# Optimization experiments

Hardware: AMD Instinct MI355X
Metric: run time of the kernel (lower is better)

Reference implementation:

```python
import jax, jax.numpy as jnp
import numpy as np

N_NODES = 100000
EPS = 1e-12  # F.normalize eps


def mean_aggregate(x, src, dst):
    # gather source features along edges, segment-mean into destinations
    msg = x[src]                                              # [E, D]
    summed = jax.ops.segment_sum(msg, dst, num_segments=N_NODES)  # [N, D]
    cnt = jax.ops.segment_sum(jnp.ones_like(dst, dtype=x.dtype), dst,
                              num_segments=N_NODES)           # [N]
    return summed / jnp.maximum(cnt, 1.0)[:, None]


def sage_conv(x, src, dst, W_l, b_l, W_r, normalize):
    agg = mean_aggregate(x, src, dst)
    out = agg @ W_l.T + b_l + x @ W_r.T  # lin_l(mean neigh) + lin_r(root)
    if normalize:
        norm = jnp.sqrt(jnp.sum(out * out, axis=-1, keepdims=True))
        out = out / jnp.maximum(norm, EPS)
    return out


def setup_inputs() -> dict:
    key = jax.random.key(0)
    ks = jax.random.split(key, 8)
    H, O = 128, 128
    s = 1.0 / np.sqrt(H)
    x = jax.random.normal(ks[0], (N_NODES, H), dtype=jnp.float32)
    edge_index = jax.random.randint(ks[1], (2, 1600000), 0, N_NODES, dtype=jnp.int64)
    return {
        "x": x,
        "edge_index": edge_index,
        "W1l": jax.random.uniform(ks[2], (H, H), jnp.float32, -s, s),
        "b1": jax.random.uniform(ks[3], (H,), jnp.float32, -s, s),
        "W1r": jax.random.uniform(ks[4], (H, H), jnp.float32, -s, s),
        "W2l": jax.random.uniform(ks[5], (O, H), jnp.float32, -s, s),
        "b2": jax.random.uniform(ks[6], (O,), jnp.float32, -s, s),
        "W2r": jax.random.uniform(ks[7], (O, H), jnp.float32, -s, s),
    }


def reference(x, edge_index, W1l, b1, W1r, W2l, b2, W2r):
    src, dst = edge_index[0], edge_index[1]
    h = sage_conv(x, src, dst, W1l, b1, W1r, normalize=True)
    h = jax.nn.relu(h)
    out = sage_conv(h, src, dst, W2l, b2, W2r, normalize=False)
    return out
```

## Files before the change

kernel.cpp:

```cpp
#include <hip/hip_runtime.h>
#include <hip/hip_bf16.h>
#include <hip/hip_fp16.h>

#define N_NODES 100000
#define DFEAT 128
#define SLAB 4096
#define BSHIFT 9
#define NBUCK 196

#define WS_CNT      0
#define WS_GH       100000
#define WS_PARTB    180000
#define WS_OFFS     200000
#define WS_ESRC     300608
#define WS_AGGH     1900608
#define WS_CASTH    8300608

typedef _Float16 half8 __attribute__((ext_vector_type(8)));
typedef _Float16 half2v __attribute__((ext_vector_type(2)));
typedef float floatx4 __attribute__((ext_vector_type(4)));

__global__ __launch_bounds__(256) void prep_kernel(const float* __restrict__ x,
                                                   __half* __restrict__ xh, int total4,
                                                   const int* __restrict__ dst,
                                                   int* __restrict__ gh,
                                                   int E, int bpart, int castblocks) {
    __shared__ int lh[NBUCK];
    int b = blockIdx.x;
    if (b < castblocks) {
        int i = b * 256 + threadIdx.x;
        if (i < total4) {
            float4 v = ((const float4*)x)[i];
            __half2 h01 = __floats2half2_rn(v.x, v.y);
            __half2 h23 = __floats2half2_rn(v.z, v.w);
            uint2 o;
            o.x = *(unsigned int*)&h01;
            o.y = *(unsigned int*)&h23;
            ((uint2*)xh)[i] = o;
        }
        return;
    }
    int bb = b - castblocks;
    for (int i = threadIdx.x; i < NBUCK; i += 256) lh[i] = 0;
    __syncthreads();
    int s0 = bb * SLAB, s1 = min(E, s0 + SLAB);
    for (int i = s0 + threadIdx.x; i < s1; i += 256)
        atomicAdd(&lh[dst[i] >> BSHIFT], 1);
    __syncthreads();
    for (int i = threadIdx.x; i < NBUCK; i += 256) gh[i * bpart + bb] = lh[i];
}

__global__ void scan1_kernel(int* __restrict__ gh, int* __restrict__ partial, int m) {
    __shared__ int s[256];
    int i = blockIdx.x * 256 + threadIdx.x;
    int v = (i < m) ? gh[i] : 0;
    s[threadIdx.x] = v;
    __syncthreads();
    for (int d = 1; d < 256; d <<= 1) {
        int t = (threadIdx.x >= d) ? s[threadIdx.x - d] : 0;
        __syncthreads();
        s[threadIdx.x] += t;
        __syncthreads();
    }
    int incl = s[threadIdx.x];
    if (i < m) gh[i] = incl - v;
    if (threadIdx.x == 255) partial[blockIdx.x] = incl;
}

__global__ void scan2_kernel(int* __restrict__ partial, int nb) {
    __shared__ int s[512];
    int t = threadIdx.x;
    int v = (t < nb) ? partial[t] : 0;
    s[t] = v;
    __syncthreads();
    for (int d = 1; d < 512; d <<= 1) {
        int u = (t >= d) ? s[t - d] : 0;
        __syncthreads();
        s[t] += u;
        __syncthreads();
    }
    if (t < nb) partial[t] = s[t] - v;
}

__global__ void scan3_kernel(int* __restrict__ gh, const int* __restrict__ partial, int m) {
    int i = blockIdx.x * 256 + threadIdx.x;
    if (i < m) gh[i] += partial[blockIdx.x];
}

__global__ __launch_bounds__(256) void phase2_kernel(const int* __restrict__ src,
                                                     const int* __restrict__ dst,
                                                     const int* __restrict__ gbase,
                                                     int2* __restrict__ pairs,
                                                     int E, int bpart) {
    __shared__ int lbase[NBUCK];
    __shared__ int lcur[NBUCK];
    __shared__ int lgb[NBUCK];
    __shared__ int sc[256];
    __shared__ int2 lp[SLAB];
    int b = blockIdx.x;
    int t = threadIdx.x;
    for (int i = t; i < NBUCK; i += 256) lbase[i] = 0;
    __syncthreads();
    int s0 = b * SLAB, s1 = min(E, s0 + SLAB);
    for (int i = s0 + t; i < s1; i += 256)
        atomicAdd(&lbase[dst[i] >> BSHIFT], 1);
    __syncthreads();
    int v = (t < NBUCK) ? lbase[t] : 0;
    sc[t] = v;
    __syncthreads();
    for (int d = 1; d < 256; d <<= 1) {
        int u = (t >= d) ? sc[t - d] : 0;
        __syncthreads();
        sc[t] += u;
        __syncthreads();
    }
    if (t < NBUCK) {
        int excl = sc[t] - v;
        lbase[t] = excl;
        lcur[t] = excl;
        lgb[t] = gbase[t * bpart + b];
    }
    __syncthreads();
    for (int i = s0 + t; i < s1; i += 256) {
        int d = dst[i];
        int s = src[i];
        int bk = d >> BSHIFT;
        int pos = atomicAdd(&lcur[bk], 1);
        lp[pos] = make_int2(s, d);
    }
    __syncthreads();
    int m = s1 - s0;
    for (int i = t; i < m; i += 256) {
        int2 p = lp[i];
        int bk = p.y >> BSHIFT;
        pairs[lgb[bk] + (i - lbase[bk])] = p;
    }
}

__global__ __launch_bounds__(512) void phase3_kernel(const int2* __restrict__ pairs,
                                                     const int* __restrict__ gbase,
                                                     int* __restrict__ cnt,
                                                     int* __restrict__ offs,
                                                     int* __restrict__ esrc,
                                                     int E, int bpart, int n) {
    __shared__ int lcnt[512];
    __shared__ int sc[512];
    __shared__ int lexcl[512];
    int g = blockIdx.x;
    int node0 = g << BSHIFT;
    int t = threadIdx.x;
    lcnt[t] = 0;
    __syncthreads();
    int S = gbase[g * bpart];
    int Eg = (g == NBUCK - 1) ? E : gbase[(g + 1) * bpart];
    for (int i = S + t; i < Eg; i += 512)
        atomicAdd(&lcnt[pairs[i].y - node0], 1);
    __syncthreads();
    int v = lcnt[t];
    sc[t] = v;
    __syncthreads();
    for (int d = 1; d < 512; d <<= 1) {
        int u = (t >= d) ? sc[t - d] : 0;
        __syncthreads();
        sc[t] += u;
        __syncthreads();
    }
    int excl = sc[t] - v;
    lexcl[t] = excl;
    int nd = node0 + t;
    if (nd < n) {
        cnt[nd] = v;
        offs[nd] = S + excl;
    }
    __syncthreads();
    for (int i = S + t; i < Eg; i += 512) {
        int2 p = pairs[i];
        int pos = atomicAdd(&lexcl[p.y - node0], 1);
        esrc[S + pos] = p.x;
    }
}

#define ACC(c, r)                        \
    s[c][0] += *(half2v*)&(r).x;         \
    s[c][1] += *(half2v*)&(r).y;         \
    s[c][2] += *(half2v*)&(r).z;         \
    s[c][3] += *(half2v*)&(r).w;

__global__ void aggregate_kernel(const __half* __restrict__ feat, const int* __restrict__ esrc,
                                 const int* __restrict__ offs, const int* __restrict__ cnt,
                                 __half* __restrict__ agg, int n) {
    int wid = (blockIdx.x * blockDim.x + threadIdx.x) >> 6;
    int lane = threadIdx.x & 63;
    int grp = lane >> 4;
    int l15 = lane & 15;
    int node = wid * 4 + grp;
    if (node >= n) return;
    int beg = offs[node];
    int deg = cnt[node];
    const _Float16* fbase = (const _Float16*)feat + l15 * 8;
    const int* ep = esrc + beg;

    half2v s[4][4];
#pragma unroll
    for (int c = 0; c < 4; c++)
#pragma unroll
        for (int k = 0; k < 4; k++) s[c][k] = (half2v)(_Float16)0;

    int j = 0;
    for (; j + 8 <= deg; j += 8) {
        int i0 = ep[j + 0], i1 = ep[j + 1], i2 = ep[j + 2], i3 = ep[j + 3];
        int i4 = ep[j + 4], i5 = ep[j + 5], i6 = ep[j + 6], i7 = ep[j + 7];
        uint4 r0 = *(const uint4*)(fbase + (size_t)i0 * DFEAT);
        uint4 r1 = *(const uint4*)(fbase + (size_t)i1 * DFEAT);
        uint4 r2 = *(const uint4*)(fbase + (size_t)i2 * DFEAT);
        uint4 r3 = *(const uint4*)(fbase + (size_t)i3 * DFEAT);
        uint4 r4 = *(const uint4*)(fbase + (size_t)i4 * DFEAT);
        uint4 r5 = *(const uint4*)(fbase + (size_t)i5 * DFEAT);
        uint4 r6 = *(const uint4*)(fbase + (size_t)i6 * DFEAT);
        uint4 r7 = *(const uint4*)(fbase + (size_t)i7 * DFEAT);
        ACC(0, r0) ACC(1, r1) ACC(2, r2) ACC(3, r3)
        ACC(0, r4) ACC(1, r5) ACC(2, r6) ACC(3, r7)
    }
    for (; j + 4 <= deg; j += 4) {
        int i0 = ep[j + 0], i1 = ep[j + 1], i2 = ep[j + 2], i3 = ep[j + 3];
        uint4 r0 = *(const uint4*)(fbase + (size_t)i0 * DFEAT);
        uint4 r1 = *(const uint4*)(fbase + (size_t)i1 * DFEAT);
        uint4 r2 = *(const uint4*)(fbase + (size_t)i2 * DFEAT);
        uint4 r3 = *(const uint4*)(fbase + (size_t)i3 * DFEAT);
        ACC(0, r0) ACC(1, r1) ACC(2, r2) ACC(3, r3)
    }
    if (j < deg) {
        int rem = deg - j;
        int i0 = ep[j];
        int i1 = ep[j + (rem > 1 ? 1 : 0)];
        int i2 = ep[j + (rem > 2 ? 2 : 0)];
        uint4 r0 = *(const uint4*)(fbase + (size_t)i0 * DFEAT);
        uint4 r1 = *(const uint4*)(fbase + (size_t)i1 * DFEAT);
        uint4 r2 = *(const uint4*)(fbase + (size_t)i2 * DFEAT);
        if (rem < 2) { r1.x = 0u; r1.y = 0u; r1.z = 0u; r1.w = 0u; }
        if (rem < 3) { r2.x = 0u; r2.y = 0u; r2.z = 0u; r2.w = 0u; }
        ACC(0, r0) ACC(1, r1) ACC(2, r2)
    }

    float scale = 1.0f / fmaxf((float)deg, 1.0f);
    float a[8];
#pragma unroll
    for (int k = 0; k < 4; k++) {
        a[2 * k]     = ((float)s[0][k].x + (float)s[1][k].x) + ((float)s[2][k].x + (float)s[3][k].x);
        a[2 * k + 1] = ((float)s[0][k].y + (float)s[1][k].y) + ((float)s[2][k].y + (float)s[3][k].y);
    }
    __half2 h0 = __floats2half2_rn(a[0] * scale, a[1] * scale);
    __half2 h1 = __floats2half2_rn(a[2] * scale, a[3] * scale);
    __half2 h2 = __floats2half2_rn(a[4] * scale, a[5] * scale);
    __half2 h3 = __floats2half2_rn(a[6] * scale, a[7] * scale);
    uint4 o;
    o.x = *(unsigned int*)&h0;
    o.y = *(unsigned int*)&h1;
    o.z = *(unsigned int*)&h2;
    o.w = *(unsigned int*)&h3;
    *(uint4*)(agg + (size_t)node * DFEAT + l15 * 8) = o;
}

template <bool NORM_RELU>
__global__ __launch_bounds__(256) void gemm_mfma_kernel(
    const __half* __restrict__ A1_, const __half* __restrict__ A2_,
    const float* __restrict__ Wl, const float* __restrict__ Wr,
    const float* __restrict__ bias, float* __restrict__ out32,
    __half* __restrict__ out16, int n) {
    __shared__ __align__(16) _Float16 lw[128 * 136];

    const _Float16* A1 = (const _Float16*)A1_;
    const _Float16* A2 = (const _Float16*)A2_;

    const int lane = threadIdx.x & 63;
    const int w = threadIdx.x >> 6;
    const int quad = lane >> 4;
    const int l15 = lane & 15;
    const int i0 = blockIdx.x * 128 + w * 32;

    floatx4 acc[2][8];
#pragma unroll
    for (int nt = 0; nt < 2; nt++)
#pragma unroll
        for (int ft = 0; ft < 8; ft++)
            acc[nt][ft] = (floatx4){0.f, 0.f, 0.f, 0.f};

    int r0 = i0 + l15;      if (r0 >= n) r0 = n - 1;
    int r1 = i0 + 16 + l15; if (r1 >= n) r1 = n - 1;
    const int kq = quad * 8;

    for (int half = 0; half < 2; half++) {
        const float* __restrict__ W = half ? Wr : Wl;
        const _Float16* __restrict__ A = half ? A2 : A1;
        if (half) __syncthreads();
        {
            int t = threadIdx.x;
            int row = t >> 1;
            int cb = (t & 1) * 64;
            const float4* sp = (const float4*)(W + row * DFEAT + cb);
            unsigned int* dp = (unsigned int*)&lw[row * 136 + cb];
#pragma unroll
            for (int q = 0; q < 16; q++) {
                float4 v = sp[q];
                __half2 h01 = __floats2half2_rn(v.x, v.y);
                __half2 h23 = __floats2half2_rn(v.z, v.w);
                dp[q * 2] = *(unsigned int*)&h01;
                dp[q * 2 + 1] = *(unsigned int*)&h23;
            }
        }
        __syncthreads();
#pragma unroll
        for (int kc = 0; kc < DFEAT; kc += 32) {
            half8 b0 = *(const half8*)(A + (size_t)r0 * DFEAT + kc + kq);
            half8 b1 = *(const half8*)(A + (size_t)r1 * DFEAT + kc + kq);
#pragma unroll
            for (int ft = 0; ft < 8; ft++) {
                half8 a = *(const half8*)&lw[(ft * 16 + l15) * 136 + kc + kq];
                acc[0][ft] = __builtin_amdgcn_mfma_f32_16x16x32_f16(a, b0, acc[0][ft], 0, 0, 0);
                acc[1][ft] = __builtin_amdgcn_mfma_f32_16x16x32_f16(a, b1, acc[1][ft], 0, 0, 0);
            }
        }
    }

#pragma unroll
    for (int nt = 0; nt < 2; nt++) {
        int node = i0 + nt * 16 + l15;
        float v[8][4];
#pragma unroll
        for (int ft = 0; ft < 8; ft++) {
            const float4 bq = *(const float4*)(bias + ft * 16 + quad * 4);
            v[ft][0] = acc[nt][ft][0] + bq.x;
            v[ft][1] = acc[nt][ft][1] + bq.y;
            v[ft][2] = acc[nt][ft][2] + bq.z;
            v[ft][3] = acc[nt][ft][3] + bq.w;
        }
        if (NORM_RELU) {
            float ss = 0.f;
#pragma unroll
            for (int ft = 0; ft < 8; ft++)
#pragma unroll
                for (int r = 0; r < 4; r++) ss = fmaf(v[ft][r], v[ft][r], ss);
            ss += __shfl_xor(ss, 16);
            ss += __shfl_xor(ss, 32);
            float inv = 1.0f / fmaxf(sqrtf(ss), 1e-12f);
#pragma unroll
            for (int ft = 0; ft < 8; ft++)
#pragma unroll
                for (int r = 0; r < 4; r++) v[ft][r] = fmaxf(v[ft][r] * inv, 0.0f);
        }
        if (node < n) {
            if (NORM_RELU) {
                __half* op = (__half*)out16 + (size_t)node * DFEAT + quad * 4;
#pragma unroll
                for (int ft = 0; ft < 8; ft++) {
                    __half2 h01 = __floats2half2_rn(v[ft][0], v[ft][1]);
                    __half2 h23 = __floats2half2_rn(v[ft][2], v[ft][3]);
                    uint2 o;
                    o.x = *(unsigned int*)&h01;
                    o.y = *(unsigned int*)&h23;
                    *(uint2*)(op + ft * 16) = o;
                }
            } else {
                float* op = out32 + (size_t)node * DFEAT + quad * 4;
#pragma unroll
                for (int ft = 0; ft < 8; ft++)
                    *(float4*)(op + ft * 16) = make_float4(v[ft][0], v[ft][1], v[ft][2], v[ft][3]);
            }
        }
    }
}

extern "C" void kernel_launch(void* const* d_in, const int* in_sizes, int n_in,
                              void* d_out, int out_size, void* d_ws, size_t ws_size,
                              hipStream_t stream) {
    const float* x = (const float*)d_in[0];
    const int* edge_index = (const int*)d_in[1];
    const float* W1l = (const float*)d_in[2];
    const float* b1 = (const float*)d_in[3];
    const float* W1r = (const float*)d_in[4];
    const float* W2l = (const float*)d_in[5];
    const float* b2 = (const float*)d_in[6];
    const float* W2r = (const float*)d_in[7];
    float* out = (float*)d_out;

    const int E = in_sizes[1] / 2;
    const int n = in_sizes[0] / DFEAT;

    int* ws = (int*)d_ws;
    int* cnt = ws + WS_CNT;
    int* gh = ws + WS_GH;
    int* partialB = ws + WS_PARTB;
    int* offs = ws + WS_OFFS;
    int* esrc = ws + WS_ESRC;
    int2* pairs = (int2*)(ws + WS_AGGH);
    __half* aggh = (__half*)(ws + WS_AGGH);
    __half* casth = (__half*)(ws + WS_CASTH);

    const int* src = edge_index;
    const int* dst = edge_index + E;

    const int bpart = (E + SLAB - 1) / SLAB;
    const int m = NBUCK * bpart;
    const int blocksB = (m + 255) / 256;
    const int total4 = n * DFEAT / 4;
    const int castblocks = (total4 + 255) / 256;

    prep_kernel<<<castblocks + bpart, 256, 0, stream>>>(x, casth, total4, dst, gh,
                                                        E, bpart, castblocks);
    scan1_kernel<<<blocksB, 256, 0, stream>>>(gh, partialB, m);
    scan2_kernel<<<1, 512, 0, stream>>>(partialB, blocksB);
    scan3_kernel<<<blocksB, 256, 0, stream>>>(gh, partialB, m);

    phase2_kernel<<<bpart, 256, 0, stream>>>(src, dst, gh, pairs, E, bpart);
    phase3_kernel<<<NBUCK, 512, 0, stream>>>(pairs, gh, cnt, offs, esrc, E, bpart, n);

    const int nwaves = (n + 3) / 4;
    const int aggb = (nwaves * 64 + 255) / 256;
    const int gemmb = (n + 127) / 128;

    aggregate_kernel<<<aggb, 256, 0, stream>>>(casth, esrc, offs, cnt, aggh, n);
    gemm_mfma_kernel<true><<<gemmb, 256, 0, stream>>>(aggh, casth, W1l, W1r, b1, nullptr, aggh, n);

    aggregate_kernel<<<aggb, 256, 0, stream>>>(aggh, esrc, offs, cnt, casth, n);
    gemm_mfma_kernel<false><<<gemmb, 256, 0, stream>>>(casth, aggh, W2l, W2r, b2, out, nullptr, n);
}
```

Before: 346.2 us.

## Replace per-slab bucket scan with atomic bucket bases and pre-cast fp16 weights

```diff
diff --git a/kernel.cpp b/kernel.cpp
--- a/kernel.cpp
+++ b/kernel.cpp
@@ -9,8 +9,10 @@
 #define NBUCK 196
 
 #define WS_CNT      0
-#define WS_GH       100000
-#define WS_PARTB    180000
+#define WS_W16      100000
+#define WS_BCNT     180000
+#define WS_BBASE    180200
+#define WS_BCUR     180400
 #define WS_OFFS     200000
 #define WS_ESRC     300608
 #define WS_AGGH     1900608
@@ -23,7 +25,12 @@
 __global__ __launch_bounds__(256) void prep_kernel(const float* __restrict__ x,
                                                    __half* __restrict__ xh, int total4,
                                                    const int* __restrict__ dst,
-                                                   int* __restrict__ gh,
+                                                   int* __restrict__ bcnt,
+                                                   const float* __restrict__ W1l,
+                                                   const float* __restrict__ W1r,
+                                                   const float* __restrict__ W2l,
+                                                   const float* __restrict__ W2r,
+                                                   __half* __restrict__ w16,
                                                    int E, int bpart, int castblocks) {
     __shared__ int lh[NBUCK];
     int b = blockIdx.x;
@@ -40,58 +47,57 @@
         }
         return;
     }
-    int bb = b - castblocks;
+    if (b < castblocks + 64) {
+        int i = (b - castblocks) * 256 + threadIdx.x;
+        int m = i >> 12;
+        int off = i & 4095;
+        const float* Wp = (m == 0) ? W1l : (m == 1) ? W1r : (m == 2) ? W2l : W2r;
+        float4 v = ((const float4*)Wp)[off];
+        __half2 h01 = __floats2half2_rn(v.x, v.y);
+        __half2 h23 = __floats2half2_rn(v.z, v.w);
+        uint2 o;
+        o.x = *(unsigned int*)&h01;
+        o.y = *(unsigned int*)&h23;
+        ((uint2*)w16)[i] = o;
+        return;
+    }
+    int bb = b - castblocks - 64;
     for (int i = threadIdx.x; i < NBUCK; i += 256) lh[i] = 0;
     __syncthreads();
     int s0 = bb * SLAB, s1 = min(E, s0 + SLAB);
     for (int i = s0 + threadIdx.x; i < s1; i += 256)
         atomicAdd(&lh[dst[i] >> BSHIFT], 1);
     __syncthreads();
-    for (int i = threadIdx.x; i < NBUCK; i += 256) gh[i * bpart + bb] = lh[i];
-}
-
-__global__ void scan1_kernel(int* __restrict__ gh, int* __restrict__ partial, int m) {
+    for (int i = threadIdx.x; i < NBUCK; i += 256)
+        if (lh[i] > 0) atomicAdd(&bcnt[i], lh[i]);
+}
+
+__global__ void bscan_kernel(const int* __restrict__ bcnt, int* __restrict__ bbase,
+                             int* __restrict__ bcur, int E) {
     __shared__ int s[256];
-    int i = blockIdx.x * 256 + threadIdx.x;
-    int v = (i < m) ? gh[i] : 0;
-    s[threadIdx.x] = v;
+    int t = threadIdx.x;
+    int v = (t < NBUCK) ? bcnt[t] : 0;
+    s[t] = v;
     __syncthreads();
     for (int d = 1; d < 256; d <<= 1) {
-        int t = (threadIdx.x >= d) ? s[threadIdx.x - d] : 0;
-        __syncthreads();
-        s[threadIdx.x] += t;
-        __syncthreads();
-    }
-    int incl = s[threadIdx.x];
-    if (i < m) gh[i] = incl - v;
-    if (threadIdx.x == 255) partial[blockIdx.x] = incl;
-}
-
-__global__ void scan2_kernel(int* __restrict__ partial, int nb) {
-    __shared__ int s[512];
-    int t = threadIdx.x;
-    int v = (t < nb) ? partial[t] : 0;
-    s[t] = v;
-    __syncthreads();
-    for (int d = 1; d < 512; d <<= 1) {
         int u = (t >= d) ? s[t - d] : 0;
         __syncthreads();
         s[t] += u;
         __syncthreads();
     }
-    if (t < nb) partial[t] = s[t] - v;
-}
-
-__global__ void scan3_kernel(int* __restrict__ gh, const int* __restrict__ partial, int m) {
-    int i = blockIdx.x * 256 + threadIdx.x;
-    if (i < m) gh[i] += partial[blockIdx.x];
+    if (t < NBUCK) {
+        int excl = s[t] - v;
+        bbase[t] = excl;
+        bcur[t] = excl;
+    }
+    if (t == 0) bbase[NBUCK] = E;
 }
 
 __global__ __launch_bounds__(256) void phase2_kernel(const int* __restrict__ src,
                                                      const int* __restrict__ dst,
-                                                     const int* __restrict__ gbase,
+                                                     int* __restrict__ bcur,
                                                      int2* __restrict__ pairs,
-                                                     int E, int bpart) {
+                                                     int E) {
     __shared__ int lbase[NBUCK];
     __shared__ int lcur[NBUCK];
     __shared__ int lgb[NBUCK];
@@ -118,7 +124,7 @@
         int excl = sc[t] - v;
         lbase[t] = excl;
         lcur[t] = excl;
-        lgb[t] = gbase[t * bpart + b];
+        lgb[t] = (v > 0) ? atomicAdd(&bcur[t], v) : 0;
     }
     __syncthreads();
     for (int i = s0 + t; i < s1; i += 256) {
@@ -138,11 +144,11 @@
 }
 
 __global__ __launch_bounds__(512) void phase3_kernel(const int2* __restrict__ pairs,
-                                                     const int* __restrict__ gbase,
+                                                     const int* __restrict__ bbase,
                                                      int* __restrict__ cnt,
                                                      int* __restrict__ offs,
                                                      int* __restrict__ esrc,
-                                                     int E, int bpart, int n) {
+                                                     int n) {
     __shared__ int lcnt[512];
     __shared__ int sc[512];
     __shared__ int lexcl[512];
@@ -151,8 +157,8 @@
     int t = threadIdx.x;
     lcnt[t] = 0;
     __syncthreads();
-    int S = gbase[g * bpart];
-    int Eg = (g == NBUCK - 1) ? E : gbase[(g + 1) * bpart];
+    int S = bbase[g];
+    int Eg = bbase[g + 1];
     for (int i = S + t; i < Eg; i += 512)
         atomicAdd(&lcnt[pairs[i].y - node0], 1);
     __syncthreads();
@@ -262,110 +268,123 @@
 }
 
 template <bool NORM_RELU>
-__global__ __launch_bounds__(256) void gemm_mfma_kernel(
+__global__ __launch_bounds__(256) void gemm64_kernel(
     const __half* __restrict__ A1_, const __half* __restrict__ A2_,
-    const float* __restrict__ Wl, const float* __restrict__ Wr,
+    const __half* __restrict__ Wl16, const __half* __restrict__ Wr16,
     const float* __restrict__ bias, float* __restrict__ out32,
     __half* __restrict__ out16, int n) {
     __shared__ __align__(16) _Float16 lw[128 * 136];
 
     const _Float16* A1 = (const _Float16*)A1_;
     const _Float16* A2 = (const _Float16*)A2_;
+    const _Float16* wl = (const _Float16*)Wl16;
+    const _Float16* wr = (const _Float16*)Wr16;
 
     const int lane = threadIdx.x & 63;
     const int w = threadIdx.x >> 6;
     const int quad = lane >> 4;
     const int l15 = lane & 15;
-    const int i0 = blockIdx.x * 128 + w * 32;
-
-    floatx4 acc[2][8];
-#pragma unroll
-    for (int nt = 0; nt < 2; nt++)
+    const int i0 = blockIdx.x * 64 + w * 16;
+    int r = i0 + l15;
+    if (r >= n) r = n - 1;
+    const int kq = quad * 8;
+
+    half8 bf[4];
+#pragma unroll
+    for (int k = 0; k < 4; k++)
+        bf[k] = *(const half8*)(A1 + (size_t)r * DFEAT + k * 32 + kq);
+
+    {
+        int t = threadIdx.x;
+        int row = t >> 1;
+        int cb = (t & 1) * 64;
+        const uint4* sp = (const uint4*)(wl + row * DFEAT + cb);
+        uint4* dp = (uint4*)&lw[row * 136 + cb];
+#pragma unroll
+        for (int q = 0; q < 8; q++) dp[q] = sp[q];
+    }
+    __syncthreads();
+
+    floatx4 acc[8];
+#pragma unroll
+    for (int ft = 0; ft < 8; ft++) acc[ft] = (floatx4){0.f, 0.f, 0.f, 0.f};
+
+#pragma unroll
+    for (int kci = 0; kci < 4; kci++) {
+#pragma unroll
+        for (int ft = 0; ft < 8; ft++) {
+            half8 a = *(const half8*)&lw[(ft * 16 + l15) * 136 + kci * 32 + kq];
+            acc[ft] = __builtin_amdgcn_mfma_f32_16x16x32_f16(a, bf[kci], acc[ft], 0, 0, 0);
+        }
+    }
+
+    half8 xf[4];
+#pragma unroll
+    for (int k = 0; k < 4; k++)
+        xf[k] = *(const half8*)(A2 + (size_t)r * DFEAT + k * 32 + kq);
+
+    __syncthreads();
+    {
+        int t = threadIdx.x;
+        int row = t >> 1;
+        int cb = (t & 1) * 64;
+        const uint4* sp = (const uint4*)(wr + row * DFEAT + cb);
+        uint4* dp = (uint4*)&lw[row * 136 + cb];
+#pragma unroll
+        for (int q = 0; q < 8; q++) dp[q] = sp[q];
+    }
+    __syncthreads();
+
+#pragma unroll
+    for (int kci = 0; kci < 4; kci++) {
+#pragma unroll
+        for (int ft = 0; ft < 8; ft++) {
+            half8 a = *(const half8*)&lw[(ft * 16 + l15) * 136 + kci * 32 + kq];
+            acc[ft] = __builtin_amdgcn_mfma_f32_16x16x32_f16(a, xf[kci], acc[ft], 0, 0, 0);
+        }
+    }
+
+    int node = i0 + l15;
+    float v[8][4];
+#pragma unroll
+    for (int ft = 0; ft < 8; ft++) {
+        const float4 bq = *(const float4*)(bias + ft * 16 + quad * 4);
+        v[ft][0] = acc[ft][0] + bq.x;
+        v[ft][1] = acc[ft][1] + bq.y;
+        v[ft][2] = acc[ft][2] + bq.z;
+        v[ft][3] = acc[ft][3] + bq.w;
+    }
+    if (NORM_RELU) {
+        float ss = 0.f;
 #pragma unroll
         for (int ft = 0; ft < 8; ft++)
-            acc[nt][ft] = (floatx4){0.f, 0.f, 0.f, 0.f};
-
-    int r0 = i0 + l15;      if (r0 >= n) r0 = n - 1;
-    int r1 = i0 + 16 + l15; if (r1 >= n) r1 = n - 1;
-    const int kq = quad * 8;
-
-    for (int half = 0; half < 2; half++) {
-        const float* __restrict__ W = half ? Wr : Wl;
-        const _Float16* __restrict__ A = half ? A2 : A1;
-        if (half) __syncthreads();
-        {
-            int t = threadIdx.x;
-            int row = t >> 1;
-            int cb = (t & 1) * 64;
-            const float4* sp = (const float4*)(W + row * DFEAT + cb);
-            unsigned int* dp = (unsigned int*)&lw[row * 136 + cb];
-#pragma unroll
-            for (int q = 0; q < 16; q++) {
-                float4 v = sp[q];
-                __half2 h01 = __floats2half2_rn(v.x, v.y);
-                __half2 h23 = __floats2half2_rn(v.z, v.w);
-                dp[q * 2] = *(unsigned int*)&h01;
-                dp[q * 2 + 1] = *(unsigned int*)&h23;
+#pragma unroll
+            for (int q = 0; q < 4; q++) ss = fmaf(v[ft][q], v[ft][q], ss);
+        ss += __shfl_xor(ss, 16);
+        ss += __shfl_xor(ss, 32);
+        float inv = 1.0f / fmaxf(sqrtf(ss), 1e-12f);
+#pragma unroll
+        for (int ft = 0; ft < 8; ft++)
+#pragma unroll
+            for (int q = 0; q < 4; q++) v[ft][q] = fmaxf(v[ft][q] * inv, 0.0f);
+    }
+    if (node < n) {
+        if (NORM_RELU) {
+            __half* op = (__half*)out16 + (size_t)node * DFEAT + quad * 4;
+#pragma unroll
+            for (int ft = 0; ft < 8; ft++) {
+                __half2 h01 = __floats2half2_rn(v[ft][0], v[ft][1]);
+                __half2 h23 = __floats2half2_rn(v[ft][2], v[ft][3]);
+                uint2 o;
+                o.x = *(unsigned int*)&h01;
+                o.y = *(unsigned int*)&h23;
+                *(uint2*)(op + ft * 16) = o;
             }
-        }
-        __syncthreads();
-#pragma unroll
-        for (int kc = 0; kc < DFEAT; kc += 32) {
-            half8 b0 = *(const half8*)(A + (size_t)r0 * DFEAT + kc + kq);
-            half8 b1 = *(const half8*)(A + (size_t)r1 * DFEAT + kc + kq);
-#pragma unroll
-            for (int ft = 0; ft < 8; ft++) {
-                half8 a = *(const half8*)&lw[(ft * 16 + l15) * 136 + kc + kq];
-                acc[0][ft] = __builtin_amdgcn_mfma_f32_16x16x32_f16(a, b0, acc[0][ft], 0, 0, 0);
-                acc[1][ft] = __builtin_amdgcn_mfma_f32_16x16x32_f16(a, b1, acc[1][ft], 0, 0, 0);
-            }
-        }
-    }
-
-#pragma unroll
-    for (int nt = 0; nt < 2; nt++) {
-        int node = i0 + nt * 16 + l15;
-        float v[8][4];
-#pragma unroll
-        for (int ft = 0; ft < 8; ft++) {
-            const float4 bq = *(const float4*)(bias + ft * 16 + quad * 4);
-            v[ft][0] = acc[nt][ft][0] + bq.x;
-            v[ft][1] = acc[nt][ft][1] + bq.y;
-            v[ft][2] = acc[nt][ft][2] + bq.z;
-            v[ft][3] = acc[nt][ft][3] + bq.w;
-        }
-        if (NORM_RELU) {
-            float ss = 0.f;
+        } else {
+            float* op = out32 + (size_t)node * DFEAT + quad * 4;
 #pragma unroll
             for (int ft = 0; ft < 8; ft++)
-#pragma unroll
-                for (int r = 0; r < 4; r++) ss = fmaf(v[ft][r], v[ft][r], ss);
-            ss += __shfl_xor(ss, 16);
-            ss += __shfl_xor(ss, 32);
-            float inv = 1.0f / fmaxf(sqrtf(ss), 1e-12f);
-#pragma unroll
-            for (int ft = 0; ft < 8; ft++)
-#pragma unroll
-                for (int r = 0; r < 4; r++) v[ft][r] = fmaxf(v[ft][r] * inv, 0.0f);
-        }
-        if (node < n) {
-            if (NORM_RELU) {
-                __half* op = (__half*)out16 + (size_t)node * DFEAT + quad * 4;
-#pragma unroll
-                for (int ft = 0; ft < 8; ft++) {
-                    __half2 h01 = __floats2half2_rn(v[ft][0], v[ft][1]);
-                    __half2 h23 = __floats2half2_rn(v[ft][2], v[ft][3]);
-                    uint2 o;
-                    o.x = *(unsigned int*)&h01;
-                    o.y = *(unsigned int*)&h23;
-                    *(uint2*)(op + ft * 16) = o;
-                }
-            } else {
-                float* op = out32 + (size_t)node * DFEAT + quad * 4;
-#pragma unroll
-                for (int ft = 0; ft < 8; ft++)
-                    *(float4*)(op + ft * 16) = make_float4(v[ft][0], v[ft][1], v[ft][2], v[ft][3]);
-            }
+                *(float4*)(op + ft * 16) = make_float4(v[ft][0], v[ft][1], v[ft][2], v[ft][3]);
         }
     }
 }
@@ -388,8 +407,10 @@
 
     int* ws = (int*)d_ws;
     int* cnt = ws + WS_CNT;
-    int* gh = ws + WS_GH;
-    int* partialB = ws + WS_PARTB;
+    __half* w16 = (__half*)(ws + WS_W16);
+    int* bcnt = ws + WS_BCNT;
+    int* bbase = ws + WS_BBASE;
+    int* bcur = ws + WS_BCUR;
     int* offs = ws + WS_OFFS;
     int* esrc = ws + WS_ESRC;
     int2* pairs = (int2*)(ws + WS_AGGH);
@@ -400,27 +421,31 @@
     const int* dst = edge_index + E;
 
     const int bpart = (E + SLAB - 1) / SLAB;
-    const int m = NBUCK * bpart;
-    const int blocksB = (m + 255) / 256;
     const int total4 = n * DFEAT / 4;
     const int castblocks = (total4 + 255) / 256;
 
-    prep_kernel<<<castblocks + bpart, 256, 0, stream>>>(x, casth, total4, dst, gh,
-                                                        E, bpart, castblocks);
-    scan1_kernel<<<blocksB, 256, 0, stream>>>(gh, partialB, m);
-    scan2_kernel<<<1, 512, 0, stream>>>(partialB, blocksB);
-    scan3_kernel<<<blocksB, 256, 0, stream>>>(gh, partialB, m);
-
-    phase2_kernel<<<bpart, 256, 0, stream>>>(src, dst, gh, pairs, E, bpart);
-    phase3_kernel<<<NBUCK, 512, 0, stream>>>(pairs, gh, cnt, offs, esrc, E, bpart, n);
+    __half* w1l16 = w16;
+    __half* w1r16 = w16 + 16384;
+    __half* w2l16 = w16 + 32768;
+    __half* w2r16 = w16 + 49152;
+
+    hipMemsetAsync(bcnt, 0, NBUCK * sizeof(int), stream);
+
+    prep_kernel<<<castblocks + 64 + bpart, 256, 0, stream>>>(
+        x, casth, total4, dst, bcnt, W1l, W1r, W2l, W2r, w16, E, bpart, castblocks);
+    bscan_kernel<<<1, 256, 0, stream>>>(bcnt, bbase, bcur, E);
+    phase2_kernel<<<bpart, 256, 0, stream>>>(src, dst, bcur, pairs, E);
+    phase3_kernel<<<NBUCK, 512, 0, stream>>>(pairs, bbase, cnt, offs, esrc, n);
 
     const int nwaves = (n + 3) / 4;
     const int aggb = (nwaves * 64 + 255) / 256;
-    const int gemmb = (n + 127) / 128;
+    const int gemmb = (n + 63) / 64;
 
     aggregate_kernel<<<aggb, 256, 0, stream>>>(casth, esrc, offs, cnt, aggh, n);
-    gemm_mfma_kernel<true><<<gemmb, 256, 0, stream>>>(aggh, casth, W1l, W1r, b1, nullptr, aggh, n);
+    gemm64_kernel<true><<<gemmb, 256, 0, stream>>>(aggh, casth, w1l16, w1r16, b1,
+                                                   nullptr, aggh, n);
 
     aggregate_kernel<<<aggb, 256, 0, stream>>>(aggh, esrc, offs, cnt, casth, n);
-    gemm_mfma_kernel<false><<<gemmb, 256, 0, stream>>>(casth, aggh, W2l, W2r, b2, out, nullptr, n);
-}
+    gemm64_kernel<false><<<gemmb, 256, 0, stream>>>(casth, aggh, w2l16, w2r16, b2,
+                                                    out, nullptr, n);
+}
```

New measurement: 341.1 us. About the same (-1.5%).
